# Performance work log

Measured on AMD Instinct MI355X. Metric: run time of the kernel, lower is better.

## Reference

```python
import jax, jax.numpy as jnp
import numpy as np
from jax import lax

EPS = 1e-5
DN = ('NCHW', 'OIHW', 'NCHW')


def setup_inputs() -> dict:
    key = jax.random.key(0)
    ks = jax.random.split(key, 16)
    B = 8192
    # uniform(0,1): every pixel nonzero => all voxels active => sparse conv == dense conv
    x = jax.random.uniform(ks[0], (B, 1, 28, 28), dtype=jnp.float32)

    def conv_params(kw, kb, c_in, c_out, k):
        scale = 1.0 / np.sqrt(c_in * k * k)
        w = jax.random.normal(kw, (c_out, c_in, k, k), dtype=jnp.float32) * scale
        b = jax.random.normal(kb, (c_out,), dtype=jnp.float32) * scale
        return w, b

    w0, b0 = conv_params(ks[1], ks[2], 1, 32, 3)
    w1, b1 = conv_params(ks[3], ks[4], 32, 64, 2)
    w2, b2 = conv_params(ks[5], ks[6], 64, 128, 2)
    # BatchNorm affine params (init: gamma=1, beta=0)
    g0, be0 = jnp.ones((32,), jnp.float32), jnp.zeros((32,), jnp.float32)
    g1, be1 = jnp.ones((64,), jnp.float32), jnp.zeros((64,), jnp.float32)
    g2, be2 = jnp.ones((128,), jnp.float32), jnp.zeros((128,), jnp.float32)
    w_fc = jax.random.normal(ks[7], (10, 128), dtype=jnp.float32) * (1.0 / np.sqrt(128))
    b_fc = jax.random.normal(ks[8], (10,), dtype=jnp.float32) * (1.0 / np.sqrt(128))
    return dict(x=x, w0=w0, b0=b0, g0=g0, be0=be0,
                w1=w1, b1=b1, g1=g1, be1=be1,
                w2=w2, b2=b2, g2=g2, be2=be2,
                w_fc=w_fc, b_fc=b_fc)


def _conv_bn_relu(x, w, b, g, be, stride, padding):
    # sparse conv on fully-active grid == dense conv
    y = lax.conv_general_dilated(x, w, (stride, stride), padding,
                                 dimension_numbers=DN)
    y = y + b[None, :, None, None]
    # BatchNorm1d over (N_active, C) == stats over batch+spatial (biased var)
    mean = jnp.mean(y, axis=(0, 2, 3))
    var = jnp.var(y, axis=(0, 2, 3))
    y = (y - mean[None, :, None, None]) * lax.rsqrt(var + EPS)[None, :, None, None]
    y = y * g[None, :, None, None] + be[None, :, None, None]
    return jax.nn.relu(y)


def reference(x, w0, b0, g0, be0, w1, b1, g1, be1, w2, b2, g2, be2, w_fc, b_fc):
    h = _conv_bn_relu(x, w0, b0, g0, be0, 1, 'SAME')    # (B,32,28,28)
    h = _conv_bn_relu(h, w1, b1, g1, be1, 2, 'VALID')   # (B,64,14,14)
    h = _conv_bn_relu(h, w2, b2, g2, be2, 2, 'VALID')   # (B,128,7,7)
    pooled = jnp.mean(h, axis=(2, 3))                    # AdaptiveAvgPool2d(1)+Flatten
    return pooled @ w_fc.T + b_fc                        # (B, n_classes)
```

## Files before the change

kernel.cpp:

```cpp
#include <hip/hip_runtime.h>
#include <hip/hip_bf16.h>

typedef __bf16 bf16x8 __attribute__((ext_vector_type(8)));
typedef float  f32x4  __attribute__((ext_vector_type(4)));

#define BSZ 8192

union BW2 { __bf16 b[2]; unsigned int u; };
union FR  { unsigned int u[4]; bf16x8 v; };

__global__ __launch_bounds__(256) void k_stats0(const float* __restrict__ x,
                                                float* __restrict__ part0,
                                                const float* __restrict__ w1,
                                                const float* __restrict__ w2,
                                                __bf16* __restrict__ w1b,
                                                __bf16* __restrict__ w2b) {
    __shared__ float sred[4 * 54];
    const int tid = threadIdx.x;
    {
        int t = blockIdx.x * 256 + tid;
        if (t < 8192) {
            int oc = t >> 7, k = t & 127, c = k & 31, d = k >> 5;
            w1b[t] = (__bf16)w1[oc * 128 + c * 4 + d];
        }
        if (t < 32768) {
            int oc = t >> 8, k = t & 255, c = k & 63, d = k >> 6;
            w2b[t] = (__bf16)w2[oc * 256 + c * 4 + d];
        }
    }
    float a[54];
#pragma unroll
    for (int i = 0; i < 54; i++) a[i] = 0.f;
    const int total = BSZ * 784;
    for (int p = blockIdx.x * 256 + tid; p < total; p += gridDim.x * 256) {
        int b = p / 784, pix = p - b * 784;
        int y = pix / 28, xx = pix - y * 28;
        const float* xb = x + (long)b * 784;
        float nv[9];
#pragma unroll
        for (int dy = 0; dy < 3; dy++) {
            int yy = y + dy - 1;
#pragma unroll
            for (int dx = 0; dx < 3; dx++) {
                int x2 = xx + dx - 1;
                nv[dy * 3 + dx] = (yy >= 0 && yy < 28 && x2 >= 0 && x2 < 28) ? xb[yy * 28 + x2] : 0.f;
            }
        }
        int idx = 0;
#pragma unroll
        for (int t2 = 0; t2 < 9; t2++) {
            float vt = nv[t2];
            a[45 + t2] += vt;
#pragma unroll
            for (int u = t2; u < 9; u++) { a[idx] += vt * nv[u]; idx++; }
        }
    }
#pragma unroll
    for (int i = 0; i < 54; i++) {
        float v = a[i];
        v += __shfl_xor(v, 1);  v += __shfl_xor(v, 2);  v += __shfl_xor(v, 4);
        v += __shfl_xor(v, 8);  v += __shfl_xor(v, 16); v += __shfl_xor(v, 32);
        a[i] = v;
    }
    const int l = tid & 63, w = tid >> 6;
    if (l == 0) {
#pragma unroll
        for (int i = 0; i < 54; i++) sred[w * 54 + i] = a[i];
    }
    __syncthreads();
    if (tid < 54)
        part0[blockIdx.x * 64 + tid] = sred[tid] + sred[54 + tid] + sred[108 + tid] + sred[162 + tid];
}

__global__ void k_fin0(const float* __restrict__ part0, const float* __restrict__ w0,
                       const float* __restrict__ g0, const float* __restrict__ be0,
                       __bf16* __restrict__ wcv) {
    __shared__ float red[4 * 54];
    int t = threadIdx.x, c = t & 63, g = t >> 6;
    if (c < 54) {
        float acc = 0.f;
        for (int i = g; i < 1008; i += 4) acc += part0[i * 64 + c];
        red[g * 54 + c] = acc;
    }
    __syncthreads();
    if (t < 54) red[t] = red[t] + red[54 + t] + red[108 + t] + red[162 + t];
    __syncthreads();
    if (t < 32) {
        float wv[9];
#pragma unroll
        for (int tap = 0; tap < 9; tap++) wv[tap] = w0[t * 9 + tap];
        float sum = 0.f, sq = 0.f;
        int idx = 0;
#pragma unroll
        for (int ta = 0; ta < 9; ta++) {
            sum = fmaf(wv[ta], red[45 + ta], sum);
#pragma unroll
            for (int u = ta; u < 9; u++) {
                float coef = (u == ta) ? 1.f : 2.f;
                sq = fmaf(coef * wv[ta] * wv[u], red[idx], sq);
                idx++;
            }
        }
        float cnt = (float)BSZ * 784.f;
        float mean = sum / cnt;
        float var = sq / cnt - mean * mean;
        float A = g0[t] * rsqrtf(var + 1e-5f);
        float bias = be0[t] - mean * A;
        __bf16 bhi = (__bf16)bias;
        float blo = bias - (float)bhi;
        int nn = t >> 1, hh = t & 1;
#pragma unroll
        for (int qq = 0; qq < 4; qq++) {
#pragma unroll
            for (int e = 0; e < 8; e++) {
                float v = 0.f;
                if (qq < 3) {
                    if (e < 6) {
                        int i = e >> 1;
                        v = (float)((__bf16)(A * wv[qq * 3 + i]));
                    } else if (e == 6) {
                        float wf = A * wv[qq * 3 + 0]; v = wf - (float)((__bf16)wf);
                    } else {
                        float wf = A * wv[qq * 3 + 1]; v = wf - (float)((__bf16)wf);
                    }
                } else {
                    if (e == 0)      { float wf = A * wv[2]; v = wf - (float)((__bf16)wf); }
                    else if (e == 1) { float wf = A * wv[5]; v = wf - (float)((__bf16)wf); }
                    else if (e == 2) { float wf = A * wv[8]; v = wf - (float)((__bf16)wf); }
                    else if (e == 4) v = (float)bhi;
                    else if (e == 5) v = blo;
                }
                wcv[hh * 512 + qq * 128 + nn * 8 + e] = (__bf16)v;
            }
        }
    }
}

struct C0S {
    bf16x8 bwM0, bwM1;
    int q, n;
    int Koff, off1, off2;
    bool q3;
};

__device__ inline void c0_init(C0S& S, const __bf16* __restrict__ wcv, int l) {
    S.q = l >> 4; S.n = l & 15; S.q3 = (S.q == 3);
    S.bwM0 = *(const bf16x8*)&wcv[S.q * 128 + S.n * 8];
    S.bwM1 = *(const bf16x8*)&wcv[512 + S.q * 128 + S.n * 8];
    S.Koff = S.q3 ? 2 : S.q * 30;
    S.off1 = S.q3 ? 30 : 1;
    S.off2 = S.q3 ? 60 : 2;
}

__device__ inline void c0_produce(const C0S& S, const unsigned* __restrict__ xs2w,
                                  __bf16* sAtw, int my, int mx, bool zpad) {
    const int b00 = 2 * my * 30 + 2 * mx + S.Koff;
#pragma unroll
    for (int t = 0; t < 4; t++) {
        const int d1 = t >> 1, d0 = t & 1;
        const unsigned* p = xs2w + b00 + d1 * 30 + d0;
        unsigned v0 = p[0], v1 = p[S.off1], v2 = p[S.off2];
        unsigned pm = __builtin_amdgcn_perm(v1, v0, 0x05040100u);
        FR A;
        A.u[0] = S.q3 ? pm : v0;
        A.u[1] = S.q3 ? (v2 & 0xffffu) : v1;
        A.u[2] = S.q3 ? 0x3F803F80u : v2;
        A.u[3] = S.q3 ? 0u : pm;
        f32x4 z = {0.f, 0.f, 0.f, 0.f};
        f32x4 ac0 = __builtin_amdgcn_mfma_f32_16x16x32_bf16(A.v, S.bwM0, z, 0, 0, 0);
        f32x4 ac1 = __builtin_amdgcn_mfma_f32_16x16x32_bf16(A.v, S.bwM1, z, 0, 0, 0);
#pragma unroll
        for (int r = 0; r < 4; r++) {
            float a0 = fmaxf(ac0[r], 0.f), a1 = fmaxf(ac1[r], 0.f);
            if (zpad) { a0 = 0.f; a1 = 0.f; }
            BW2 pk; pk.b[0] = (__bf16)a0; pk.b[1] = (__bf16)a1;
            *(unsigned*)&sAtw[(S.q * 4 + r) * 136 + t * 32 + 2 * S.n] = pk.u;
        }
    }
}

__device__ inline void stage_img(unsigned* xs2w, const float* __restrict__ x,
                                 long b, int t0, int stride) {
    for (int jj = t0; jj < 784; jj += stride) {
        int yy = jj / 28, xx2 = jj - yy * 28;
        float f = x[b * 784 + jj];
        __bf16 hi = (__bf16)f;
        __bf16 lo = (__bf16)(f - (float)hi);
        BW2 pk; pk.b[0] = hi; pk.b[1] = lo;
        xs2w[(yy + 1) * 30 + xx2 + 1] = pk.u;
    }
}

__global__ __launch_bounds__(256, 4) void k_conv01(const float* __restrict__ x,
                                                   const __bf16* __restrict__ wcv,
                                                   const __bf16* __restrict__ w1b,
                                                   __bf16* __restrict__ h1,
                                                   float* __restrict__ part1) {
    __shared__ unsigned xs2a[4][900];
    __shared__ __attribute__((aligned(16))) __bf16 sAta[4][16 * 136];
    const int tid = threadIdx.x, w = tid >> 6, l = tid & 63;
    const int q = l >> 4, n = l & 15;
    unsigned* xs2w = xs2a[w];
    __bf16* sAtw = sAta[w];
    C0S S0; c0_init(S0, wcv, l);
    bf16x8 fbv[4][4];
#pragma unroll
    for (int g = 0; g < 4; g++)
#pragma unroll
        for (int kc = 0; kc < 4; kc++)
            fbv[g][kc] = *(const bf16x8*)&w1b[(4 * n + g) * 128 + kc * 32 + q * 8];
    const long b = (long)blockIdx.x * 4 + w;
    for (int i = l; i < 900; i += 64) xs2w[i] = 0u;
    stage_img(xs2w, x, b, l, 64);
    float ssum[4] = {0.f, 0.f, 0.f, 0.f}, ssq[4] = {0.f, 0.f, 0.f, 0.f};
    __bf16* hb = h1 + b * 12544;
    for (int mt = 0; mt < 13; mt++) {
        const bool last = (mt == 12);
        int mv = (last && n >= 4) ? 195 : mt * 16 + n;
        int my = mv / 14, mx = mv - my * 14;
        c0_produce(S0, xs2w, sAtw, my, mx, last && (q != 0));
        const __bf16* sa = &sAtw[n * 136 + q * 8];
        bf16x8 fav[4];
#pragma unroll
        for (int kc = 0; kc < 4; kc++) fav[kc] = *(const bf16x8*)&sa[kc * 32];
        f32x4 a[4];
        __builtin_amdgcn_s_setprio(1);
#pragma unroll
        for (int g = 0; g < 4; g++) {
            f32x4 acc = {0.f, 0.f, 0.f, 0.f};
#pragma unroll
            for (int kc = 0; kc < 4; kc++)
                acc = __builtin_amdgcn_mfma_f32_16x16x32_bf16(fav[kc], fbv[g][kc], acc, 0, 0, 0);
            a[g] = acc;
        }
        __builtin_amdgcn_s_setprio(0);
#pragma unroll
        for (int g = 0; g < 4; g++)
#pragma unroll
            for (int r = 0; r < 4; r++) {
                ssum[g] += a[g][r];
                ssq[g] = fmaf(a[g][r], a[g][r], ssq[g]);
            }
        if ((mt < 12) | (q == 0)) {
#pragma unroll
            for (int r = 0; r < 4; r++) {
                BW2 p0, p1;
                p0.b[0] = (__bf16)a[0][r]; p0.b[1] = (__bf16)a[1][r];
                p1.b[0] = (__bf16)a[2][r]; p1.b[1] = (__bf16)a[3][r];
                uint2 u; u.x = p0.u; u.y = p1.u;
                *(uint2*)&hb[(mt * 16 + q * 4 + r) * 64 + 4 * n] = u;
            }
        }
    }
#pragma unroll
    for (int g = 0; g < 4; g++) {
        ssum[g] += __shfl_xor(ssum[g], 16); ssum[g] += __shfl_xor(ssum[g], 32);
        ssq[g]  += __shfl_xor(ssq[g], 16);  ssq[g]  += __shfl_xor(ssq[g], 32);
    }
    if (l < 16) {
#pragma unroll
        for (int g = 0; g < 4; g++) {
            part1[(long)(4 * l + g) * BSZ + b] = ssum[g];
            part1[(long)(64 + 4 * l + g) * BSZ + b] = ssq[g];
        }
    }
}

__global__ __launch_bounds__(256) void k_redfin(const float* __restrict__ part,
                                                const float* __restrict__ g,
                                                const float* __restrict__ be,
                                                float* __restrict__ abc,
                                                int C, float cnt) {
    __shared__ float s1[256], s2[256];
    const int c = blockIdx.x, tid = threadIdx.x;
    float a = 0.f, bq = 0.f;
    const float* p1 = part + (long)c * BSZ;
    const float* p2 = part + (long)(C + c) * BSZ;
    for (int i = tid; i < BSZ; i += 256) { a += p1[i]; bq += p2[i]; }
    s1[tid] = a; s2[tid] = bq;
    __syncthreads();
    for (int s = 128; s > 0; s >>= 1) {
        if (tid < s) { s1[tid] += s1[tid + s]; s2[tid] += s2[tid + s]; }
        __syncthreads();
    }
    if (tid == 0) {
        float mean = s1[0] / cnt;
        float var = s2[0] / cnt - mean * mean;
        float A = g[c] * rsqrtf(var + 1e-5f);
        abc[c] = A;
        abc[C + c] = be[c] - mean * A;
    }
}

__global__ __launch_bounds__(256) void k_conv2s(__bf16* __restrict__ h1,
                                                const __bf16* __restrict__ w2b,
                                                const float* __restrict__ abc1,
                                                float* __restrict__ part2) {
    __shared__ __attribute__((aligned(16))) __bf16 sAt[2][16 * 264];
    __shared__ float sbn1[128];
    const int tid = threadIdx.x;
    if (tid < 128) sbn1[tid] = abc1[tid];
    const int w = tid >> 6, l = tid & 63, q = l >> 4, n = l & 15;
    bf16x8 fbv[2][8];
#pragma unroll
    for (int ntl = 0; ntl < 2; ntl++) {
        int oc = w * 32 + 2 * n + ntl;
#pragma unroll
        for (int kc = 0; kc < 8; kc++)
            fbv[ntl][kc] = *(const bf16x8*)&w2b[oc * 256 + kc * 32 + q * 8];
    }
    const int rlA = tid >> 5, rlB = 8 + (tid >> 5), oo = (tid & 31) * 8;
    const int dA = oo >> 6, cA = oo & 63;

    auto issue = [&](int li, bf16x8& A0, bf16x8& A1) {
        const int img = li >> 2, mt = li & 3;
        const __bf16* src = h1 + ((long)blockIdx.x * 4 + img) * 12544;
        int r0 = mt * 16 + rlA;
        if (r0 < 49) {
            int py = r0 / 7, px = r0 - py * 7;
            int msrc = (2 * py + (dA >> 1)) * 14 + 2 * px + (dA & 1);
            A0 = *(const bf16x8*)&src[msrc * 64 + cA];
        }
        int r1 = mt * 16 + rlB;
        if (r1 < 49) {
            int py = r1 / 7, px = r1 - py * 7;
            int msrc = (2 * py + (dA >> 1)) * 14 + 2 * px + (dA & 1);
            A1 = *(const bf16x8*)&src[msrc * 64 + cA];
        }
    };
    auto put = [&](int li, bf16x8 A0, bf16x8 A1) {
        const int mt = li & 3;
        __bf16* sb = sAt[li & 1];
        bf16x8 wv;
        if (mt * 16 + rlA < 49) {
#pragma unroll
            for (int j = 0; j < 8; j++)
                wv[j] = (__bf16)fmaxf((float)A0[j] * sbn1[cA + j] + sbn1[64 + cA + j], 0.f);
        } else {
#pragma unroll
            for (int j = 0; j < 8; j++) wv[j] = (__bf16)0.0f;
        }
        *(bf16x8*)&sb[rlA * 264 + oo] = wv;
        if (mt * 16 + rlB < 49) {
#pragma unroll
            for (int j = 0; j < 8; j++)
                wv[j] = (__bf16)fmaxf((float)A1[j] * sbn1[cA + j] + sbn1[64 + cA + j], 0.f);
        } else {
#pragma unroll
            for (int j = 0; j < 8; j++) wv[j] = (__bf16)0.0f;
        }
        *(bf16x8*)&sb[rlB * 264 + oo] = wv;
    };

    bf16x8 cur0 = {}, cur1 = {}, nxt0 = {}, nxt1 = {};
    issue(0, cur0, cur1);
    __syncthreads();
    float ssum[2] = {0.f, 0.f}, ssq[2] = {0.f, 0.f};
    for (int li = 0; li < 16; li++) {
        const int img = li >> 2, mt = li & 3;
        put(li, cur0, cur1);
        if (li < 15) issue(li + 1, nxt0, nxt1);
        __builtin_amdgcn_sched_barrier(0);
        asm volatile("s_waitcnt lgkmcnt(0)" ::: "memory");
        __builtin_amdgcn_s_barrier();
        __builtin_amdgcn_sched_barrier(0);
        const __bf16* sb = sAt[li & 1];
        bf16x8 fav[8];
#pragma unroll
        for (int kc = 0; kc < 8; kc++)
            fav[kc] = *(const bf16x8*)&sb[n * 264 + kc * 32 + q * 8];
        f32x4 accA = {0.f, 0.f, 0.f, 0.f}, accB = {0.f, 0.f, 0.f, 0.f};
        __builtin_amdgcn_s_setprio(1);
#pragma unroll
        for (int kc = 0; kc < 8; kc++) {
            accA = __builtin_amdgcn_mfma_f32_16x16x32_bf16(fav[kc], fbv[0][kc], accA, 0, 0, 0);
            accB = __builtin_amdgcn_mfma_f32_16x16x32_bf16(fav[kc], fbv[1][kc], accB, 0, 0, 0);
        }
        __builtin_amdgcn_s_setprio(0);
        __bf16* src = h1 + ((long)blockIdx.x * 4 + img) * 12544;
#pragma unroll
        for (int rr = 0; rr < 4; rr++) {
            int m = mt * 16 + q * 4 + rr;
            BW2 pk; pk.b[0] = (__bf16)accA[rr]; pk.b[1] = (__bf16)accB[rr];
            if (m < 49) *(unsigned int*)&src[m * 128 + w * 32 + 2 * n] = pk.u;
            ssum[0] += accA[rr]; ssq[0] = fmaf(accA[rr], accA[rr], ssq[0]);
            ssum[1] += accB[rr]; ssq[1] = fmaf(accB[rr], accB[rr], ssq[1]);
        }
        cur0 = nxt0; cur1 = nxt1;
        if (mt == 3) {
            const long b = (long)blockIdx.x * 4 + img;
#pragma unroll
            for (int ntl = 0; ntl < 2; ntl++) {
                ssum[ntl] += __shfl_xor(ssum[ntl], 16); ssum[ntl] += __shfl_xor(ssum[ntl], 32);
                ssq[ntl]  += __shfl_xor(ssq[ntl], 16);  ssq[ntl]  += __shfl_xor(ssq[ntl], 32);
            }
            if (l < 16) {
#pragma unroll
                for (int ntl = 0; ntl < 2; ntl++) {
                    int oc = w * 32 + 2 * l + ntl;
                    part2[(long)oc * BSZ + b] = ssum[ntl];
                    part2[(long)(128 + oc) * BSZ + b] = ssq[ntl];
                }
            }
            ssum[0] = ssum[1] = ssq[0] = ssq[1] = 0.f;
        }
    }
}

__global__ __launch_bounds__(256) void k_final(const __bf16* __restrict__ z2,
                                               const float* __restrict__ abc2,
                                               const float* __restrict__ wfc,
                                               const float* __restrict__ bfc,
                                               float* __restrict__ out) {
    const int tid = threadIdx.x, w = tid >> 6, l = tid & 63;
    const int q = l >> 4, g = l & 15;
    const long b = (long)blockIdx.x * 4 + w;
    const __bf16* src = z2 + b * 12544;
    f32x4 a2lo = *(const f32x4*)&abc2[g * 8];
    f32x4 a2hi = *(const f32x4*)&abc2[g * 8 + 4];
    f32x4 b2lo = *(const f32x4*)&abc2[128 + g * 8];
    f32x4 b2hi = *(const f32x4*)&abc2[128 + g * 8 + 4];
    float acc[8];
#pragma unroll
    for (int j = 0; j < 8; j++) acc[j] = 0.f;
    for (int r = q; r < 49; r += 4) {
        bf16x8 v = *(const bf16x8*)&src[r * 128 + g * 8];
#pragma unroll
        for (int j = 0; j < 4; j++) {
            acc[j]     += fmaxf((float)v[j]     * a2lo[j] + b2lo[j], 0.f);
            acc[4 + j] += fmaxf((float)v[4 + j] * a2hi[j] + b2hi[j], 0.f);
        }
    }
#pragma unroll
    for (int j = 0; j < 8; j++) {
        acc[j] += __shfl_xor(acc[j], 16);
        acc[j] += __shfl_xor(acc[j], 32);
        acc[j] *= (1.f / 49.f);
    }
    float p[10];
#pragma unroll
    for (int o = 0; o < 10; o++) {
        f32x4 w0 = *(const f32x4*)&wfc[o * 128 + g * 8];
        f32x4 w1 = *(const f32x4*)&wfc[o * 128 + g * 8 + 4];
        float s = 0.f;
#pragma unroll
        for (int j = 0; j < 4; j++) {
            s = fmaf(acc[j], w0[j], s);
            s = fmaf(acc[4 + j], w1[j], s);
        }
        p[o] = s;
    }
#pragma unroll
    for (int o = 0; o < 10; o++) {
        p[o] += __shfl_xor(p[o], 1); p[o] += __shfl_xor(p[o], 2);
        p[o] += __shfl_xor(p[o], 4); p[o] += __shfl_xor(p[o], 8);
    }
    if (l == 0) {
#pragma unroll
        for (int o = 0; o < 10; o++) out[b * 10 + o] = p[o] + bfc[o];
    }
}

extern "C" void kernel_launch(void* const* d_in, const int* in_sizes, int n_in,
                              void* d_out, int out_size, void* d_ws, size_t ws_size,
                              hipStream_t stream) {
    const float* x   = (const float*)d_in[0];
    const float* w0  = (const float*)d_in[1];
    const float* g0  = (const float*)d_in[3];
    const float* be0 = (const float*)d_in[4];
    const float* w1  = (const float*)d_in[5];
    const float* g1  = (const float*)d_in[7];
    const float* be1 = (const float*)d_in[8];
    const float* w2  = (const float*)d_in[9];
    const float* g2  = (const float*)d_in[11];
    const float* be2 = (const float*)d_in[12];
    const float* wfc = (const float*)d_in[13];
    const float* bfc = (const float*)d_in[14];
    float* out = (float*)d_out;

    float* ws    = (float*)d_ws;
    float* part0 = ws;
    __bf16* wcv  = (__bf16*)(part0 + 1008 * 64);
    float* abc0  = part0 + 1024 * 64;
    float* part1 = abc0 + 320;
    float* abc1  = part1 + 128 * BSZ;
    float* part2 = abc1 + 128;
    float* abc2  = part2 + 256 * BSZ;
    __bf16* w1b  = (__bf16*)(abc2 + 256);
    __bf16* w2b  = w1b + 8192;
    __bf16* h1   = w2b + 32768;

    k_stats0<<<dim3(1008), dim3(256), 0, stream>>>(x, part0, w1, w2, w1b, w2b);
    k_fin0<<<dim3(1), dim3(256), 0, stream>>>(part0, w0, g0, be0, wcv);
    k_conv01<<<dim3(BSZ / 4), dim3(256), 0, stream>>>(x, wcv, w1b, h1, part1);
    k_redfin<<<dim3(64), dim3(256), 0, stream>>>(part1, g1, be1, abc1, 64, (float)(BSZ * 196));
    k_conv2s<<<dim3(BSZ / 4), dim3(256), 0, stream>>>(h1, w2b, abc1, part2);
    k_redfin<<<dim3(128), dim3(256), 0, stream>>>(part2, g2, be2, abc2, 128, (float)(BSZ * 49));
    k_final<<<dim3(BSZ / 4), dim3(256), 0, stream>>>(h1, abc2, wfc, bfc, out);
}
```

Baseline: 367.6 us.

## Double-buffer conv0 tile production and deepen conv2 global prefetch to two stages

In the fused conv0+conv1 kernel, the per-warp LDS staging tile is double-buffered, so the next conv0 tile is produced before the current tile is consumed by the conv1 MFMAs. This lets LDS writes overlap with the matrix work. The conv2 kernel's global-load prefetch goes from one tile ahead to two, to hide more memory latency. In exchange, LDS use and register pressure rise, and launch bounds drop to 3 blocks per SM, which lowers occupancy. The conv0 reuse of buffer mt&1 without a barrier relies on each wave owning its buffer exclusively.

```diff
diff --git a/kernel.cpp b/kernel.cpp
--- a/kernel.cpp
+++ b/kernel.cpp
@@ -153,7 +153,7 @@
 }
 
 __device__ inline void c0_produce(const C0S& S, const unsigned* __restrict__ xs2w,
-                                  __bf16* sAtw, int my, int mx, bool zpad) {
+                                  __bf16* dst, int my, int mx, bool zpad) {
     const int b00 = 2 * my * 30 + 2 * mx + S.Koff;
 #pragma unroll
     for (int t = 0; t < 4; t++) {
@@ -174,7 +174,7 @@
             float a0 = fmaxf(ac0[r], 0.f), a1 = fmaxf(ac1[r], 0.f);
             if (zpad) { a0 = 0.f; a1 = 0.f; }
             BW2 pk; pk.b[0] = (__bf16)a0; pk.b[1] = (__bf16)a1;
-            *(unsigned*)&sAtw[(S.q * 4 + r) * 136 + t * 32 + 2 * S.n] = pk.u;
+            *(unsigned*)&dst[(S.q * 4 + r) * 136 + t * 32 + 2 * S.n] = pk.u;
         }
     }
 }
@@ -191,17 +191,16 @@
     }
 }
 
-__global__ __launch_bounds__(256, 4) void k_conv01(const float* __restrict__ x,
+__global__ __launch_bounds__(256, 3) void k_conv01(const float* __restrict__ x,
                                                    const __bf16* __restrict__ wcv,
                                                    const __bf16* __restrict__ w1b,
                                                    __bf16* __restrict__ h1,
                                                    float* __restrict__ part1) {
     __shared__ unsigned xs2a[4][900];
-    __shared__ __attribute__((aligned(16))) __bf16 sAta[4][16 * 136];
+    __shared__ __attribute__((aligned(16))) __bf16 sAta[4][2][16 * 136];
     const int tid = threadIdx.x, w = tid >> 6, l = tid & 63;
     const int q = l >> 4, n = l & 15;
     unsigned* xs2w = xs2a[w];
-    __bf16* sAtw = sAta[w];
     C0S S0; c0_init(S0, wcv, l);
     bf16x8 fbv[4][4];
 #pragma unroll
@@ -214,12 +213,18 @@
     stage_img(xs2w, x, b, l, 64);
     float ssum[4] = {0.f, 0.f, 0.f, 0.f}, ssq[4] = {0.f, 0.f, 0.f, 0.f};
     __bf16* hb = h1 + b * 12544;
-    for (int mt = 0; mt < 13; mt++) {
+
+    auto prod = [&](int mt) {
         const bool last = (mt == 12);
         int mv = (last && n >= 4) ? 195 : mt * 16 + n;
         int my = mv / 14, mx = mv - my * 14;
-        c0_produce(S0, xs2w, sAtw, my, mx, last && (q != 0));
-        const __bf16* sa = &sAtw[n * 136 + q * 8];
+        c0_produce(S0, xs2w, sAta[w][mt & 1], my, mx, last && (q != 0));
+    };
+
+    prod(0);
+    for (int mt = 0; mt < 13; mt++) {
+        if (mt < 12) prod(mt + 1);
+        const __bf16* sa = &sAta[w][mt & 1][n * 136 + q * 8];
         bf16x8 fav[4];
 #pragma unroll
         for (int kc = 0; kc < 4; kc++) fav[kc] = *(const bf16x8*)&sa[kc * 32];
@@ -244,10 +249,10 @@
         if ((mt < 12) | (q == 0)) {
 #pragma unroll
             for (int r = 0; r < 4; r++) {
-                BW2 p0, p1;
+                BW2 p0, p1v;
                 p0.b[0] = (__bf16)a[0][r]; p0.b[1] = (__bf16)a[1][r];
-                p1.b[0] = (__bf16)a[2][r]; p1.b[1] = (__bf16)a[3][r];
-                uint2 u; u.x = p0.u; u.y = p1.u;
+                p1v.b[0] = (__bf16)a[2][r]; p1v.b[1] = (__bf16)a[3][r];
+                uint2 u; u.x = p0.u; u.y = p1v.u;
                 *(uint2*)&hb[(mt * 16 + q * 4 + r) * 64 + 4 * n] = u;
             }
         }
@@ -352,14 +357,15 @@
         *(bf16x8*)&sb[rlB * 264 + oo] = wv;
     };
 
-    bf16x8 cur0 = {}, cur1 = {}, nxt0 = {}, nxt1 = {};
-    issue(0, cur0, cur1);
+    bf16x8 pA0 = {}, pA1 = {}, pB0 = {}, pB1 = {}, pC0 = {}, pC1 = {};
+    issue(0, pA0, pA1);
+    issue(1, pB0, pB1);
     __syncthreads();
     float ssum[2] = {0.f, 0.f}, ssq[2] = {0.f, 0.f};
     for (int li = 0; li < 16; li++) {
         const int img = li >> 2, mt = li & 3;
-        put(li, cur0, cur1);
-        if (li < 15) issue(li + 1, nxt0, nxt1);
+        put(li, pA0, pA1);
+        if (li < 14) issue(li + 2, pC0, pC1);
         __builtin_amdgcn_sched_barrier(0);
         asm volatile("s_waitcnt lgkmcnt(0)" ::: "memory");
         __builtin_amdgcn_s_barrier();
@@ -386,7 +392,7 @@
             ssum[0] += accA[rr]; ssq[0] = fmaf(accA[rr], accA[rr], ssq[0]);
             ssum[1] += accB[rr]; ssq[1] = fmaf(accB[rr], accB[rr], ssq[1]);
         }
-        cur0 = nxt0; cur1 = nxt1;
+        pA0 = pB0; pA1 = pB1; pB0 = pC0; pB1 = pC1;
         if (mt == 3) {
             const long b = (long)blockIdx.x * 4 + img;
 #pragma unroll
```

Result: no change. 367.9 us, median of 2 (+0.1%).
